# Performance work log

Measured on AMD Instinct MI355X. Metric: run time of the kernel, lower is better.

## Reference

```python
import jax, jax.numpy as jnp
import numpy as np

B, S, D = 2, 2048, 768
H = 12
DEPTH = D // H
DFF = 4 * D
EPS = 1e-5


def setup_inputs() -> dict:
    key = jax.random.key(0)
    ks = jax.random.split(key, 9)
    sd = 0.02
    return {
        "x": jax.random.normal(ks[0], (B, S, D), dtype=jnp.float32),
        "Wqkv": jax.random.normal(ks[1], (D, 3 * D), dtype=jnp.float32) * sd,
        "Wout": jax.random.normal(ks[2], (D, D), dtype=jnp.float32) * sd,
        "bout": jnp.zeros((D,), dtype=jnp.float32),
        "W1": jax.random.normal(ks[3], (D, DFF), dtype=jnp.float32) * sd,
        "b1": jnp.zeros((DFF,), dtype=jnp.float32),
        "W2": jax.random.normal(ks[4], (DFF, D), dtype=jnp.float32) * sd,
        "b2": jnp.zeros((D,), dtype=jnp.float32),
        "g1": jnp.ones((D,), dtype=jnp.float32),
        "be1": jnp.zeros((D,), dtype=jnp.float32),
        "g2": jnp.ones((D,), dtype=jnp.float32),
        "be2": jnp.zeros((D,), dtype=jnp.float32),
    }


def _layernorm(x, gain, bias):
    mean = jnp.mean(x, axis=-1, keepdims=True)
    var = jnp.mean(jnp.square(x - mean), axis=-1, keepdims=True)  # unbiased=False
    return gain * (x - mean) / jnp.sqrt(var + EPS) + bias


def reference(x, Wqkv, Wout, bout, W1, b1, W2, b2, g1, be1, g2, be2):
    b, s, d = x.shape
    # QKV projection (no bias), chunk into q,k,v
    qkv = jnp.einsum("bsd,de->bse", x, Wqkv)
    q, k, v = jnp.split(qkv, 3, axis=-1)
    q = q.reshape(b, s, H, DEPTH).transpose(0, 2, 1, 3)  # bhsd
    k = k.reshape(b, s, H, DEPTH).transpose(0, 2, 1, 3)
    v = v.reshape(b, s, H, DEPTH).transpose(0, 2, 1, 3)
    scores = jnp.einsum("bhqd,bhkd->bhqk", q, k) / np.sqrt(DEPTH).astype(np.float32)
    # causal mask (use_masking=True)
    causal = jnp.tril(jnp.ones((s, s), dtype=bool))
    scores = jnp.where(causal, scores, -jnp.inf)
    attn = jax.nn.softmax(scores, axis=-1)
    ctx = jnp.einsum("bhqk,bhkd->bhqd", attn, v)
    ctx = ctx.transpose(0, 2, 1, 3).reshape(b, s, d)
    attn_out = jnp.einsum("bsd,de->bse", ctx, Wout) + bout
    # residual + LN1 (dropout is identity in eval)
    h = _layernorm(x + attn_out, g1, be1)
    # FFN
    ff = jax.nn.relu(jnp.einsum("bsd,df->bsf", h, W1) + b1)
    ff = jnp.einsum("bsf,fd->bsd", ff, W2) + b2
    return _layernorm(h + ff, g2, be2)
```

## Files before the change

kernel.cpp:

```cpp
#include <hip/hip_runtime.h>


typedef __attribute__((ext_vector_type(8))) short  short8;
typedef __attribute__((ext_vector_type(4))) float  floatx4;

#define QSC 0.18033688f
#define C2  24.0f

__device__ __forceinline__ float b2f(unsigned short u) {
    return __uint_as_float(((unsigned)u) << 16);
}
__device__ __forceinline__ unsigned short f2b(float f) {
    unsigned x = __float_as_uint(f);
    return (unsigned short)((x + 0x7fffu + ((x >> 16) & 1u)) >> 16);
}
__device__ __forceinline__ void async_cp16(const void* g, void* l) {
    __builtin_amdgcn_global_load_lds((const __attribute__((address_space(1))) void*)g,
                                     (__attribute__((address_space(3))) void*)l,
                                     16, 0, 0);
}
__device__ __forceinline__ int chunk_ofs8(int qb) {
    int t = qb >> 2, rem = qb & 3;
    return (t + 1) * (2 * t + rem);
}
__device__ __forceinline__ int swz16(int row, int chunk) {
    return row * 64 + (((chunk ^ (row & 7)) & 7) << 3);
}

__global__ __launch_bounds__(256) void prep_all(
    const float* __restrict__ x,    unsigned short* __restrict__ xb,
    const float* __restrict__ Wqkv, unsigned short* __restrict__ wqkvT,
    const float* __restrict__ Wout, unsigned short* __restrict__ woutT,
    const float* __restrict__ W1,   unsigned short* __restrict__ w1T,
    const float* __restrict__ W2,   unsigned short* __restrict__ w2T)
{
    __shared__ float tile[32][33];
    int idx = blockIdx.x;
    int tx = threadIdx.x & 31, ty = threadIdx.x >> 5;
    if (idx >= 6912) {
        int i = (idx - 6912) * 256 + threadIdx.x;
        float4 v = ((const float4*)x)[i];
        ushort4 u;
        u.x = f2b(v.x); u.y = f2b(v.y); u.z = f2b(v.z); u.w = f2b(v.w);
        ((ushort4*)xb)[i] = u;
        return;
    }
    const float* W; unsigned short* Wt; int K, N, bx, by;
    if (idx < 1728)      { W = Wqkv; Wt = wqkvT; K = 768;  N = 2304; bx = idx % 72;        by = idx / 72; }
    else if (idx < 2304) { W = Wout; Wt = woutT; K = 768;  N = 768;  bx = (idx-1728) % 24; by = (idx-1728) / 24; }
    else if (idx < 4608) { W = W1;   Wt = w1T;   K = 768;  N = 3072; bx = (idx-2304) % 96; by = (idx-2304) / 96; }
    else                 { W = W2;   Wt = w2T;   K = 3072; N = 768;  bx = (idx-4608) % 24; by = (idx-4608) / 24; }
    int n0 = bx * 32, k0 = by * 32;
    for (int i = ty; i < 32; i += 8)
        tile[i][tx] = W[(size_t)(k0 + i) * N + n0 + tx];
    __syncthreads();
    for (int i = ty; i < 32; i += 8)
        Wt[(size_t)(n0 + i) * K + k0 + tx] = f2b(tile[tx][i]);
}

__global__ __launch_bounds__(256) void gemm_bf16(
    const unsigned short* __restrict__ A,
    const unsigned short* __restrict__ Bt,
    const float* __restrict__ bias,
    float* __restrict__ outF,
    unsigned short* __restrict__ outB,
    int M, int N, int K, int relu, int mode, int kslab)
{
    __shared__ unsigned short As[8192];
    __shared__ unsigned short Bs[8192];
    const int tid  = threadIdx.x;
    const int m0   = blockIdx.y * 128;
    const int n0   = blockIdx.x * 128;
    const int kz   = blockIdx.z;
    const int kbeg = kz * kslab;
    const int kend = kbeg + kslab;
    const int lane = tid & 63;
    const int wave = tid >> 6;
    const int wm   = (wave >> 1) * 64;
    const int wn   = (wave & 1) * 64;
    const int fr   = lane & 15;
    const int fq   = lane >> 4;

    floatx4 acc[4][4];
    for (int i = 0; i < 4; i++)
        for (int j = 0; j < 4; j++)
            for (int e = 0; e < 4; e++) acc[i][j][e] = 0.f;

    for (int kk = kbeg; kk < kend; kk += 64) {
        __syncthreads();
        #pragma unroll
        for (int r = 0; r < 4; ++r) {
            int c   = r * 256 + tid;
            int row = c >> 3;
            int jj  = ((c & 7) ^ (row & 7)) * 8;
            async_cp16(A  + (size_t)(m0 + row) * K + kk + jj, &As[c * 8]);
            async_cp16(Bt + (size_t)(n0 + row) * K + kk + jj, &Bs[c * 8]);
        }
        __syncthreads();

        #pragma unroll
        for (int kc = 0; kc < 2; ++kc) {
            short8 a[4], b[4];
            #pragma unroll
            for (int t = 0; t < 4; t++) a[t] = *(const short8*)&As[swz16(wm + t * 16 + fr, kc * 4 + fq)];
            #pragma unroll
            for (int t = 0; t < 4; t++) b[t] = *(const short8*)&Bs[swz16(wn + t * 16 + fr, kc * 4 + fq)];
            #pragma unroll
            for (int i = 0; i < 4; i++)
                #pragma unroll
                for (int j = 0; j < 4; j++)
                    acc[i][j] = __builtin_amdgcn_mfma_f32_16x16x32_bf16(a[i], b[j], acc[i][j], 0, 0, 0);
        }
    }

    if (mode == 2) {
        float* dst = outF + (size_t)kz * M * N;
        #pragma unroll
        for (int j = 0; j < 4; j++) {
            int col = n0 + wn + j * 16 + fr;
            #pragma unroll
            for (int i = 0; i < 4; i++) {
                int rbase = m0 + wm + i * 16 + fq * 4;
                #pragma unroll
                for (int e = 0; e < 4; e++)
                    dst[(size_t)(rbase + e) * N + col] = acc[i][j][e];
            }
        }
        return;
    }
    if (mode == 1) {
        #pragma unroll
        for (int j = 0; j < 4; j++) {
            int col   = n0 + wn + j * 16 + fr;
            int which = (col >= 1536) ? 2 : (col >= 768 ? 1 : 0);
            float sc  = (which == 0) ? QSC : 1.0f;
            int rem   = col - which * 768;
            int hh    = rem >> 6, d = rem & 63;
            #pragma unroll
            for (int i = 0; i < 4; i++) {
                int rbase = m0 + wm + i * 16 + fq * 4;
                #pragma unroll
                for (int e = 0; e < 4; e++) {
                    int row = rbase + e;
                    int b_  = row >> 11, srow = row & 2047;
                    size_t idx = (size_t)which * 3145728 +
                                 ((size_t)(b_ * 12 + hh) * 2048 + srow) * 64 + d;
                    outB[idx] = f2b(acc[i][j][e] * sc);
                }
            }
        }
        return;
    }
    #pragma unroll
    for (int j = 0; j < 4; j++) {
        int col  = n0 + wn + j * 16 + fr;
        float bv = bias ? bias[col] : 0.f;
        #pragma unroll
        for (int i = 0; i < 4; i++) {
            int rbase = m0 + wm + i * 16 + fq * 4;
            #pragma unroll
            for (int e = 0; e < 4; e++) {
                float v = acc[i][j][e] + bv;
                if (relu) v = fmaxf(v, 0.f);
                size_t idx = (size_t)(rbase + e) * N + col;
                if (outF) outF[idx] = v;
                if (outB) outB[idx] = f2b(v);
            }
        }
    }
}

__global__ __launch_bounds__(256) void attn_part(const unsigned short* __restrict__ Qg,
                                                 const unsigned short* __restrict__ Kg,
                                                 const unsigned short* __restrict__ Vg,
                                                 unsigned short* __restrict__ pO,
                                                 float* __restrict__ pL) {
    __shared__ unsigned short Ks[2][4096];
    __shared__ unsigned short Vt[2][4096];
    __shared__ unsigned short Ps[128 * 72];
    const int tid  = threadIdx.x;
    const int lane = tid & 63;
    const int wave = tid >> 6;
    const int fr   = lane & 15;
    const int fq   = lane >> 4;
    const int wm   = wave * 32;
    const int r    = 39 - blockIdx.x;
    const int bh   = blockIdx.y;
    int qb = 0;
    for (int q_ = 15; q_ >= 0; --q_) if (r >= chunk_ofs8(q_)) { qb = q_; break; }
    const int c     = r - chunk_ofs8(qb);
    const int q0    = qb * 128;
    const int tile0 = 8 * c;
    const int ntk   = min(8, 2 * (qb + 1) - 8 * c);
    const int slot  = bh * 40 + r;
    const unsigned short* Qb = Qg + (size_t)bh * 2048 * 64;
    const unsigned short* Kb = Kg + (size_t)bh * 2048 * 64;
    const unsigned short* Vb = Vg + (size_t)bh * 2048 * 64;

    short8 qf[2][2];
    #pragma unroll
    for (int rf = 0; rf < 2; ++rf) {
        const unsigned short* qr = Qb + (size_t)(q0 + wm + rf * 16 + fr) * 64;
        qf[rf][0] = *(const short8*)(qr + fq * 8);
        qf[rf][1] = *(const short8*)(qr + 32 + fq * 8);
    }

    short8 onesf;
    #pragma unroll
    for (int i = 0; i < 8; ++i) onesf[i] = (short)0x3F80;

    floatx4 o[2][4];
    floatx4 lacc[2];
    #pragma unroll
    for (int rf = 0; rf < 2; ++rf) {
        #pragma unroll
        for (int nt = 0; nt < 4; ++nt)
            #pragma unroll
            for (int e = 0; e < 4; ++e) o[rf][nt][e] = 0.f;
        #pragma unroll
        for (int e = 0; e < 4; ++e) lacc[rf][e] = 0.f;
    }

    const int c0 = tid, c1 = tid + 256;
    uint4 kr0, kr1, vr0, vr1;

#define LOADT(TG)                                                              \
    {                                                                          \
        int base = (TG) * 64;                                                  \
        kr0 = *(const uint4*)(Kb + (size_t)(base + (c0 >> 3)) * 64 + (c0 & 7) * 8); \
        kr1 = *(const uint4*)(Kb + (size_t)(base + (c1 >> 3)) * 64 + (c1 & 7) * 8); \
        vr0 = *(const uint4*)(Vb + (size_t)(base + (c0 & 63)) * 64 + (c0 >> 6) * 8); \
        vr1 = *(const uint4*)(Vb + (size_t)(base + (c1 & 63)) * 64 + (c1 >> 6) * 8); \
    }
#define WRITET(BUF)                                                            \
    {                                                                          \
        *(uint4*)&Ks[BUF][swz16(c0 >> 3, c0 & 7)] = kr0;                       \
        *(uint4*)&Ks[BUF][swz16(c1 >> 3, c1 & 7)] = kr1;                       \
        unsigned short t0[8]; *(uint4*)t0 = vr0;                               \
        _Pragma("unroll") for (int i_ = 0; i_ < 8; ++i_)                       \
            Vt[BUF][((c0 >> 6) * 8 + i_) * 64 +                                \
                    (((((c0 >> 3) & 7) ^ i_) << 3) | (c0 & 7))] = t0[i_];      \
        unsigned short t1[8]; *(uint4*)t1 = vr1;                               \
        _Pragma("unroll") for (int i_ = 0; i_ < 8; ++i_)                       \
            Vt[BUF][((c1 >> 6) * 8 + i_) * 64 +                                \
                    (((((c1 >> 3) & 7) ^ i_) << 3) | (c1 & 7))] = t1[i_];      \
    }

    LOADT(tile0);
    WRITET(0);
    __syncthreads();

    for (int kt = 0; kt < ntk; ++kt) {
        const int  tg   = tile0 + kt;
        const int  cur  = kt & 1;
        const bool more = (kt + 1 < ntk);
        if (more) LOADT(tg + 1);

        short8 kf[2][4];
        #pragma unroll
        for (int kc = 0; kc < 2; ++kc)
            #pragma unroll
            for (int nt = 0; nt < 4; ++nt)
                kf[kc][nt] = *(const short8*)&Ks[cur][swz16(nt * 16 + fr, kc * 4 + fq)];

        floatx4 s[2][4];
        #pragma unroll
        for (int rf = 0; rf < 2; ++rf)
            #pragma unroll
            for (int nt = 0; nt < 4; ++nt)
                #pragma unroll
                for (int e = 0; e < 4; ++e) s[rf][nt][e] = 0.f;
        #pragma unroll
        for (int rf = 0; rf < 2; ++rf)
            #pragma unroll
            for (int kc = 0; kc < 2; ++kc)
                #pragma unroll
                for (int nt = 0; nt < 4; ++nt)
                    s[rf][nt] = __builtin_amdgcn_mfma_f32_16x16x32_bf16(qf[rf][kc], kf[kc][nt], s[rf][nt], 0, 0, 0);

        const bool need_mask = (tg * 64 + 63) > (q0 + wm);
        #pragma unroll
        for (int rf = 0; rf < 2; ++rf) {
            const int rmin  = q0 + wm + rf * 16;
            const int pbase = (wm + rf * 16 + fq * 4) * 72 + fr;
            #pragma unroll
            for (int nt = 0; nt < 4; ++nt) {
                const bool tmask = need_mask && (tg * 64 + nt * 16 + 15 > rmin);
                const int  kvc   = tg * 64 + nt * 16 + fr;
                #pragma unroll
                for (int e = 0; e < 4; ++e) {
                    float v = s[rf][nt][e] - C2;
                    if (tmask && kvc > rmin + fq * 4 + e) v = -1e30f;
                    float pv = __builtin_amdgcn_exp2f(v);
                    Ps[pbase + e * 72 + nt * 16] =
                        (unsigned short)(__float_as_uint(pv) >> 16);
                }
            }
        }
        __asm__ volatile("s_waitcnt lgkmcnt(0)" ::: "memory");

        short8 pf[2][2], vf[2][4];
        #pragma unroll
        for (int rf = 0; rf < 2; ++rf)
            #pragma unroll
            for (int kc = 0; kc < 2; ++kc)
                pf[rf][kc] = *(const short8*)&Ps[(wm + rf * 16 + fr) * 72 + kc * 32 + fq * 8];
        #pragma unroll
        for (int kc = 0; kc < 2; ++kc)
            #pragma unroll
            for (int nt = 0; nt < 4; ++nt)
                vf[kc][nt] = *(const short8*)&Vt[cur][swz16(nt * 16 + fr, kc * 4 + fq)];
        #pragma unroll
        for (int rf = 0; rf < 2; ++rf)
            #pragma unroll
            for (int kc = 0; kc < 2; ++kc) {
                lacc[rf] = __builtin_amdgcn_mfma_f32_16x16x32_bf16(pf[rf][kc], onesf, lacc[rf], 0, 0, 0);
                #pragma unroll
                for (int nt = 0; nt < 4; ++nt)
                    o[rf][nt] = __builtin_amdgcn_mfma_f32_16x16x32_bf16(pf[rf][kc], vf[kc][nt], o[rf][nt], 0, 0, 0);
            }

        if (more) {
            WRITET(cur ^ 1);
            __syncthreads();
        }
    }
#undef LOADT
#undef WRITET

    #pragma unroll
    for (int rf = 0; rf < 2; ++rf)
        #pragma unroll
        for (int e = 0; e < 4; ++e) {
            int row = wm + rf * 16 + fq * 4 + e;
            unsigned short* orow = pO + ((size_t)slot * 128 + row) * 64;
            #pragma unroll
            for (int nt = 0; nt < 4; ++nt)
                orow[nt * 16 + fr] = f2b(o[rf][nt][e]);
            if (fr == 0)
                pL[(size_t)slot * 128 + row] = lacc[rf][e];
        }
}

__global__ __launch_bounds__(256) void attn_combine(const unsigned short* __restrict__ pO,
                                                    const float* __restrict__ pL,
                                                    unsigned short* __restrict__ ctx) {
    const int qb  = blockIdx.x;
    const int bh  = blockIdx.y;
    const int b   = bh / 12, h = bh % 12;
    const int nch = (qb >> 2) + 1;
    const int slot0 = bh * 40 + chunk_ofs8(qb);
    const int tid = threadIdx.x;
    const int row = tid >> 1;
    const int col0 = (tid & 1) * 32;

    float L = 0.f;
    for (int i = 0; i < nch; ++i)
        L += pL[(size_t)(slot0 + i) * 128 + row];

    float acc[32];
    #pragma unroll
    for (int j = 0; j < 32; ++j) acc[j] = 0.f;
    for (int i = 0; i < nch; ++i) {
        const unsigned short* p = pO + ((size_t)(slot0 + i) * 128 + row) * 64 + col0;
        #pragma unroll
        for (int v4 = 0; v4 < 4; ++v4) {
            uint4 u = *(const uint4*)(p + v4 * 8);
            unsigned short t[8]; *(uint4*)t = u;
            #pragma unroll
            for (int j = 0; j < 8; ++j) acc[v4 * 8 + j] += b2f(t[j]);
        }
    }
    float inv = 1.f / L;
    unsigned short* orow = ctx + ((size_t)(b * 2048 + qb * 128 + row)) * 768 + h * 64 + col0;
    #pragma unroll
    for (int v4 = 0; v4 < 4; ++v4) {
        unsigned short t[8];
        #pragma unroll
        for (int j = 0; j < 8; ++j) t[j] = f2b(acc[v4 * 8 + j] * inv);
        *(uint4*)(orow + v4 * 8) = *(uint4*)t;
    }
}

__global__ __launch_bounds__(256) void resid_ln2(const float* __restrict__ X,
                                                 const float* __restrict__ P,
                                                 int nsplit,
                                                 const float* __restrict__ bv,
                                                 const float* __restrict__ gain,
                                                 const float* __restrict__ beta,
                                                 float* __restrict__ outF,
                                                 unsigned short* __restrict__ outB) {
    const int row = blockIdx.x;
    const int t   = threadIdx.x;
    const size_t off = (size_t)row * 768;
    float v[3];
    #pragma unroll
    for (int i = 0; i < 3; i++) {
        size_t c = off + t + i * 256;
        float r = X[c] + bv[t + i * 256];
        for (int p = 0; p < nsplit; ++p) r += P[(size_t)p * 3145728 + c];
        v[i] = r;
    }
    float s  = v[0] + v[1] + v[2];
    float s2 = v[0] * v[0] + v[1] * v[1] + v[2] * v[2];
    #pragma unroll
    for (int o2 = 32; o2 > 0; o2 >>= 1) {
        s  += __shfl_down(s,  o2);
        s2 += __shfl_down(s2, o2);
    }
    __shared__ float rs[4], rq[4];
    if ((t & 63) == 0) { rs[t >> 6] = s; rq[t >> 6] = s2; }
    __syncthreads();
    float S    = rs[0] + rs[1] + rs[2] + rs[3];
    float S2   = rq[0] + rq[1] + rq[2] + rq[3];
    float mean = S * (1.0f / 768.0f);
    float var  = S2 * (1.0f / 768.0f) - mean * mean;
    float inv  = rsqrtf(var + 1e-5f);
    #pragma unroll
    for (int i = 0; i < 3; i++) {
        int c   = t + i * 256;
        float y = gain[c] * (v[i] - mean) * inv + beta[c];
        if (outF) outF[off + c] = y;
        if (outB) outB[off + c] = f2b(y);
    }
}

extern "C" void kernel_launch(void* const* d_in, const int* in_sizes, int n_in,
                              void* d_out, int out_size, void* d_ws, size_t ws_size,
                              hipStream_t stream) {
    const float* x    = (const float*)d_in[0];
    const float* Wqkv = (const float*)d_in[1];
    const float* Wout = (const float*)d_in[2];
    const float* bout = (const float*)d_in[3];
    const float* W1   = (const float*)d_in[4];
    const float* b1   = (const float*)d_in[5];
    const float* W2   = (const float*)d_in[6];
    const float* b2   = (const float*)d_in[7];
    const float* g1   = (const float*)d_in[8];
    const float* be1  = (const float*)d_in[9];
    const float* g2   = (const float*)d_in[10];
    const float* be2  = (const float*)d_in[11];
    float* out = (float*)d_out;

    char* ws = (char*)d_ws;
    unsigned short* wqkvT  = (unsigned short*)(ws + 0);
    unsigned short* woutT  = (unsigned short*)(ws + 3538944);
    unsigned short* w1T    = (unsigned short*)(ws + 4718592);
    unsigned short* w2T    = (unsigned short*)(ws + 9437184);
    unsigned short* xb     = (unsigned short*)(ws + 14155776);
    unsigned short* qkvG   = (unsigned short*)(ws + 20447232);
    unsigned short* Qg     = qkvG;
    unsigned short* Kg     = qkvG + 3145728;
    unsigned short* Vg     = qkvG + 6291456;
    unsigned short* pO     = (unsigned short*)(ws + 39321600);
    float*          pL     = (float*)(ws + 67633152);
    unsigned short* ctxb   = (unsigned short*)(ws + 14155776);
    float*          WoutP  = (float*)(ws + 39321600);
    float*          h      = (float*)(ws + 20447232);
    unsigned short* hb     = (unsigned short*)(ws + 77070336);
    unsigned short* ffb    = (unsigned short*)(ws + 39321600);
    float*          W2P    = (float*)(ws + 64487424);

    prep_all<<<9984, 256, 0, stream>>>(x, xb, Wqkv, wqkvT, Wout, woutT, W1, w1T, W2, w2T);
    gemm_bf16<<<dim3(18, 32), 256, 0, stream>>>(xb, wqkvT, nullptr, nullptr, qkvG,
                                                4096, 2304, 768, 0, 1, 768);
    attn_part<<<dim3(40, 24), 256, 0, stream>>>(Qg, Kg, Vg, pO, pL);
    attn_combine<<<dim3(16, 24), 256, 0, stream>>>(pO, pL, ctxb);
    gemm_bf16<<<dim3(6, 32, 3), 256, 0, stream>>>(ctxb, woutT, nullptr, WoutP, nullptr,
                                                  4096, 768, 768, 0, 2, 256);
    resid_ln2<<<4096, 256, 0, stream>>>(x, WoutP, 3, bout, g1, be1, h, hb);
    gemm_bf16<<<dim3(24, 32), 256, 0, stream>>>(hb, w1T, b1, nullptr, ffb,
                                                4096, 3072, 768, 1, 0, 768);
    gemm_bf16<<<dim3(6, 32, 2), 256, 0, stream>>>(ffb, w2T, nullptr, W2P, nullptr,
                                                  4096, 768, 3072, 0, 2, 1536);
    resid_ln2<<<4096, 256, 0, stream>>>(h, W2P, 2, b2, g2, be2, out, nullptr);
}
```

Before: 306.4 us.

## Keep attention probabilities in registers using 32x32 MFMA and permlane swap

Rewrites the attention-partial inner loop to compute S transposed (K·Q) with 32x32x16 bf16 MFMA, so P stays in registers. It is repacked with v_cvt_pk_bf16_f32 and v_permlane32_swap into the A-operand layout for the PV MFMA, which removes the LDS round trip for P and its wait. The row sum is accumulated in fp32 scalars instead of a ones-vector MFMA, and launch bounds request 4 blocks per CU. The risks are new register pressure and the correctness of the lane permutation and mask layout.

```diff
diff --git a/kernel.cpp b/kernel.cpp
--- a/kernel.cpp
+++ b/kernel.cpp
@@ -1,8 +1,10 @@
 #include <hip/hip_runtime.h>
 
 
-typedef __attribute__((ext_vector_type(8))) short  short8;
-typedef __attribute__((ext_vector_type(4))) float  floatx4;
+typedef __attribute__((ext_vector_type(8)))  short    short8;
+typedef __attribute__((ext_vector_type(4)))  float    floatx4;
+typedef __attribute__((ext_vector_type(16))) float    floatx16;
+typedef __attribute__((ext_vector_type(4)))  unsigned uint4v;
 
 #define QSC 0.18033688f
 #define C2  24.0f
@@ -18,6 +20,14 @@
     __builtin_amdgcn_global_load_lds((const __attribute__((address_space(1))) void*)g,
                                      (__attribute__((address_space(3))) void*)l,
                                      16, 0, 0);
+}
+__device__ __forceinline__ unsigned cvtpk(float lo, float hi) {
+    unsigned r;
+    asm("v_cvt_pk_bf16_f32 %0, %1, %2" : "=v"(r) : "v"(lo), "v"(hi));
+    return r;
+}
+__device__ __forceinline__ void plswap(unsigned& a, unsigned& b) {
+    asm("v_permlane32_swap_b32 %0, %1" : "+v"(a), "+v"(b));
 }
 __device__ __forceinline__ int chunk_ofs8(int qb) {
     int t = qb >> 2, rem = qb & 3;
@@ -170,19 +180,18 @@
     }
 }
 
-__global__ __launch_bounds__(256) void attn_part(const unsigned short* __restrict__ Qg,
-                                                 const unsigned short* __restrict__ Kg,
-                                                 const unsigned short* __restrict__ Vg,
-                                                 unsigned short* __restrict__ pO,
-                                                 float* __restrict__ pL) {
+__global__ __launch_bounds__(256, 4) void attn_part(const unsigned short* __restrict__ Qg,
+                                                    const unsigned short* __restrict__ Kg,
+                                                    const unsigned short* __restrict__ Vg,
+                                                    unsigned short* __restrict__ pO,
+                                                    float* __restrict__ pL) {
     __shared__ unsigned short Ks[2][4096];
     __shared__ unsigned short Vt[2][4096];
-    __shared__ unsigned short Ps[128 * 72];
     const int tid  = threadIdx.x;
     const int lane = tid & 63;
     const int wave = tid >> 6;
-    const int fr   = lane & 15;
-    const int fq   = lane >> 4;
+    const int ql   = lane & 31;
+    const int hi   = lane >> 5;
     const int wm   = wave * 32;
     const int r    = 39 - blockIdx.x;
     const int bh   = blockIdx.y;
@@ -193,33 +202,25 @@
     const int tile0 = 8 * c;
     const int ntk   = min(8, 2 * (qb + 1) - 8 * c);
     const int slot  = bh * 40 + r;
-    const unsigned short* Qb = Qg + (size_t)bh * 2048 * 64;
-    const unsigned short* Kb = Kg + (size_t)bh * 2048 * 64;
-    const unsigned short* Vb = Vg + (size_t)bh * 2048 * 64;
-
-    short8 qf[2][2];
-    #pragma unroll
-    for (int rf = 0; rf < 2; ++rf) {
-        const unsigned short* qr = Qb + (size_t)(q0 + wm + rf * 16 + fr) * 64;
-        qf[rf][0] = *(const short8*)(qr + fq * 8);
-        qf[rf][1] = *(const short8*)(qr + 32 + fq * 8);
-    }
-
-    short8 onesf;
-    #pragma unroll
-    for (int i = 0; i < 8; ++i) onesf[i] = (short)0x3F80;
-
-    floatx4 o[2][4];
-    floatx4 lacc[2];
-    #pragma unroll
-    for (int rf = 0; rf < 2; ++rf) {
-        #pragma unroll
-        for (int nt = 0; nt < 4; ++nt)
-            #pragma unroll
-            for (int e = 0; e < 4; ++e) o[rf][nt][e] = 0.f;
-        #pragma unroll
-        for (int e = 0; e < 4; ++e) lacc[rf][e] = 0.f;
-    }
+    const unsigned short* Qb = Qg + (size_t)bh * 131072;
+    const unsigned short* Kb = Kg + (size_t)bh * 131072;
+    const unsigned short* Vb = Vg + (size_t)bh * 131072;
+    const int qrow = q0 + wm + ql;
+
+    short8 qf[4];
+    {
+        const unsigned short* qr = Qb + (size_t)qrow * 64 + hi * 8;
+        #pragma unroll
+        for (int c4 = 0; c4 < 4; ++c4)
+            qf[c4] = *(const short8*)(qr + c4 * 16);
+    }
+
+    floatx16 o[2];
+    #pragma unroll
+    for (int db = 0; db < 2; ++db)
+        #pragma unroll
+        for (int e = 0; e < 16; ++e) o[db][e] = 0.f;
+    float ls[4] = {0.f, 0.f, 0.f, 0.f};
 
     const int c0 = tid, c1 = tid + 256;
     uint4 kr0, kr1, vr0, vr1;
@@ -256,69 +257,56 @@
         const bool more = (kt + 1 < ntk);
         if (more) LOADT(tg + 1);
 
-        short8 kf[2][4];
-        #pragma unroll
-        for (int kc = 0; kc < 2; ++kc)
-            #pragma unroll
-            for (int nt = 0; nt < 4; ++nt)
-                kf[kc][nt] = *(const short8*)&Ks[cur][swz16(nt * 16 + fr, kc * 4 + fq)];
-
-        floatx4 s[2][4];
-        #pragma unroll
-        for (int rf = 0; rf < 2; ++rf)
-            #pragma unroll
-            for (int nt = 0; nt < 4; ++nt)
+        #pragma unroll
+        for (int bb = 0; bb < 2; ++bb) {
+            short8 kf[4];
+            #pragma unroll
+            for (int c4 = 0; c4 < 4; ++c4)
+                kf[c4] = *(const short8*)&Ks[cur][swz16(32 * bb + ql, 2 * c4 + hi)];
+            floatx16 s;
+            #pragma unroll
+            for (int e = 0; e < 16; ++e) s[e] = 0.f;
+            #pragma unroll
+            for (int c4 = 0; c4 < 4; ++c4)
+                s = __builtin_amdgcn_mfma_f32_32x32x16_bf16(kf[c4], qf[c4], s, 0, 0, 0);
+
+            const int  kvb = tg * 64 + 32 * bb + 4 * hi;
+            const bool nm  = (tg * 64 + 32 * bb + 31) > (q0 + wm);
+            if (nm) {
                 #pragma unroll
-                for (int e = 0; e < 4; ++e) s[rf][nt][e] = 0.f;
-        #pragma unroll
-        for (int rf = 0; rf < 2; ++rf)
-            #pragma unroll
-            for (int kc = 0; kc < 2; ++kc)
-                #pragma unroll
-                for (int nt = 0; nt < 4; ++nt)
-                    s[rf][nt] = __builtin_amdgcn_mfma_f32_16x16x32_bf16(qf[rf][kc], kf[kc][nt], s[rf][nt], 0, 0, 0);
-
-        const bool need_mask = (tg * 64 + 63) > (q0 + wm);
-        #pragma unroll
-        for (int rf = 0; rf < 2; ++rf) {
-            const int rmin  = q0 + wm + rf * 16;
-            const int pbase = (wm + rf * 16 + fq * 4) * 72 + fr;
-            #pragma unroll
-            for (int nt = 0; nt < 4; ++nt) {
-                const bool tmask = need_mask && (tg * 64 + nt * 16 + 15 > rmin);
-                const int  kvc   = tg * 64 + nt * 16 + fr;
-                #pragma unroll
-                for (int e = 0; e < 4; ++e) {
-                    float v = s[rf][nt][e] - C2;
-                    if (tmask && kvc > rmin + fq * 4 + e) v = -1e30f;
-                    float pv = __builtin_amdgcn_exp2f(v);
-                    Ps[pbase + e * 72 + nt * 16] =
-                        (unsigned short)(__float_as_uint(pv) >> 16);
-                }
-            }
-        }
-        __asm__ volatile("s_waitcnt lgkmcnt(0)" ::: "memory");
-
-        short8 pf[2][2], vf[2][4];
-        #pragma unroll
-        for (int rf = 0; rf < 2; ++rf)
-            #pragma unroll
-            for (int kc = 0; kc < 2; ++kc)
-                pf[rf][kc] = *(const short8*)&Ps[(wm + rf * 16 + fr) * 72 + kc * 32 + fq * 8];
-        #pragma unroll
-        for (int kc = 0; kc < 2; ++kc)
-            #pragma unroll
-            for (int nt = 0; nt < 4; ++nt)
-                vf[kc][nt] = *(const short8*)&Vt[cur][swz16(nt * 16 + fr, kc * 4 + fq)];
-        #pragma unroll
-        for (int rf = 0; rf < 2; ++rf)
-            #pragma unroll
-            for (int kc = 0; kc < 2; ++kc) {
-                lacc[rf] = __builtin_amdgcn_mfma_f32_16x16x32_bf16(pf[rf][kc], onesf, lacc[rf], 0, 0, 0);
-                #pragma unroll
-                for (int nt = 0; nt < 4; ++nt)
-                    o[rf][nt] = __builtin_amdgcn_mfma_f32_16x16x32_bf16(pf[rf][kc], vf[kc][nt], o[rf][nt], 0, 0, 0);
-            }
+                for (int e = 0; e < 16; ++e)
+                    if (kvb + (e & 3) + 8 * (e >> 2) > qrow) s[e] = -1e30f;
+            }
+            float pv[16];
+            #pragma unroll
+            for (int e = 0; e < 16; ++e) {
+                pv[e] = __builtin_amdgcn_exp2f(s[e] - C2);
+                ls[e & 3] += pv[e];
+            }
+
+            unsigned w[8];
+            #pragma unroll
+            for (int m = 0; m < 4; ++m) {
+                w[2 * m]     = cvtpk(pv[4 * m],     pv[4 * m + 1]);
+                w[2 * m + 1] = cvtpk(pv[4 * m + 2], pv[4 * m + 3]);
+            }
+            plswap(w[0], w[2]);
+            plswap(w[1], w[3]);
+            plswap(w[4], w[6]);
+            plswap(w[5], w[7]);
+            uint4v u0 = {w[0], w[1], w[2], w[3]};
+            uint4v u1 = {w[4], w[5], w[6], w[7]};
+            short8 pa0 = __builtin_bit_cast(short8, u0);
+            short8 pa1 = __builtin_bit_cast(short8, u1);
+
+            #pragma unroll
+            for (int db = 0; db < 2; ++db) {
+                short8 vf0 = *(const short8*)&Vt[cur][swz16(32 * db + ql, 4 * bb + hi)];
+                short8 vf1 = *(const short8*)&Vt[cur][swz16(32 * db + ql, 4 * bb + 2 + hi)];
+                o[db] = __builtin_amdgcn_mfma_f32_32x32x16_bf16(pa0, vf0, o[db], 0, 0, 0);
+                o[db] = __builtin_amdgcn_mfma_f32_32x32x16_bf16(pa1, vf1, o[db], 0, 0, 0);
+            }
+        }
 
         if (more) {
             WRITET(cur ^ 1);
@@ -328,18 +316,17 @@
 #undef LOADT
 #undef WRITET
 
-    #pragma unroll
-    for (int rf = 0; rf < 2; ++rf)
-        #pragma unroll
-        for (int e = 0; e < 4; ++e) {
-            int row = wm + rf * 16 + fq * 4 + e;
-            unsigned short* orow = pO + ((size_t)slot * 128 + row) * 64;
-            #pragma unroll
-            for (int nt = 0; nt < 4; ++nt)
-                orow[nt * 16 + fr] = f2b(o[rf][nt][e]);
-            if (fr == 0)
-                pL[(size_t)slot * 128 + row] = lacc[rf][e];
-        }
+    float lsum = (ls[0] + ls[1]) + (ls[2] + ls[3]);
+    lsum += __shfl_xor(lsum, 32);
+    #pragma unroll
+    for (int db = 0; db < 2; ++db)
+        #pragma unroll
+        for (int e = 0; e < 16; ++e) {
+            int row = wm + (e & 3) + 8 * (e >> 2) + 4 * hi;
+            pO[((size_t)slot * 128 + row) * 64 + db * 32 + ql] = f2b(o[db][e]);
+        }
+    if (lane < 32)
+        pL[(size_t)slot * 128 + wm + ql] = lsum;
 }
 
 __global__ __launch_bounds__(256) void attn_combine(const unsigned short* __restrict__ pO,
```

Measured after the change: 314.1 us. +2.5%, slower.
